# Kernel tuning notes

Measured on AMD Instinct MI355X. Metric: run time of the kernel, lower is better.

The kernel has to match this reference:

```python
import jax, jax.numpy as jnp
import numpy as np

BATCH_SIZE = 2048
TEMPERATURE = 0.5
EPS = 1e-8  # torch CosineSimilarity eps


def setup_inputs() -> dict:
    key = jax.random.key(0)
    k1, k2 = jax.random.split(key)
    d = 512
    z_i = jax.random.normal(k1, (BATCH_SIZE, d), dtype=jnp.float32)
    z_j = jax.random.normal(k2, (BATCH_SIZE, d), dtype=jnp.float32)
    return {"z_i": z_i, "z_j": z_j}


def reference(z_i, z_j):
    B = BATCH_SIZE
    n = 2 * B
    z = jnp.concatenate([z_i, z_j], axis=0)              # [n, d]
    # cosine similarity via normalize + GEMM (same math as broadcasted CosineSimilarity)
    norms = jnp.maximum(jnp.linalg.norm(z, axis=1, keepdims=True), EPS)
    zn = z / norms                                       # [n, d]
    S = zn @ zn.T                                        # [n, n]
    # drop diagonal: row i keeps columns j != i, in order (matches sim[~eye].view(n, n-1))
    cols = jnp.arange(n - 1)[None, :]                    # [1, n-1]
    rows = jnp.arange(n)[:, None]                        # [n, 1]
    idx = cols + (cols >= rows)                          # skip diagonal
    off_diag = jnp.take_along_axis(S, idx, axis=1)       # [n, n-1]
    # positive pair: pos_pairs = cat(z_j, z_i) -> partner index (i + B) mod n
    pos = jnp.take_along_axis(S, ((rows[:, 0] + B) % n)[:, None], axis=1)  # [n, 1]
    logits = jnp.concatenate([pos, off_diag], axis=1) / TEMPERATURE        # [n, n]
    # cross-entropy with label 0, reduction='sum', then / n  == mean over rows
    loss = jnp.mean(jax.nn.logsumexp(logits, axis=1) - logits[:, 0])
    return loss
```

## Files before the change

kernel.cpp:

```cpp
#include <hip/hip_runtime.h>
#include <hip/hip_bf16.h>

#define N_TOT 4096
#define D     512
#define BHALF 2048

#define EXP2_SCALE 2.8853900817779268f

typedef __attribute__((ext_vector_type(8))) short short8;
typedef __attribute__((ext_vector_type(4))) float floatx4;

__global__ void normalize_kernel(const float* __restrict__ z_i,
                                 const float* __restrict__ z_j,
                                 short* __restrict__ zn) {
    int row = blockIdx.x;
    const float* src = (row < BHALF) ? (z_i + (size_t)row * D)
                                     : (z_j + (size_t)(row - BHALF) * D);
    int t = threadIdx.x;
    float4 v = ((const float4*)src)[t];
    float ss = v.x*v.x + v.y*v.y + v.z*v.z + v.w*v.w;
    for (int off = 32; off > 0; off >>= 1) ss += __shfl_down(ss, off);
    __shared__ float red[2];
    if ((t & 63) == 0) red[t >> 6] = ss;
    __syncthreads();
    float total = red[0] + red[1];
    float inv = 1.0f / fmaxf(sqrtf(total), 1e-8f);
    short4 o;
    o.x = (short)__bfloat16_as_ushort(__float2bfloat16(v.x * inv));
    o.y = (short)__bfloat16_as_ushort(__float2bfloat16(v.y * inv));
    o.z = (short)__bfloat16_as_ushort(__float2bfloat16(v.z * inv));
    o.w = (short)__bfloat16_as_ushort(__float2bfloat16(v.w * inv));
    ((short4*)(zn + (size_t)row * D))[t] = o;
}

__launch_bounds__(256)
__global__ void gemm_fused(const short* __restrict__ zn,
                           float* __restrict__ rowsum,
                           float* __restrict__ sii,
                           float* __restrict__ spos) {
    __shared__ short At[128 * 32];
    __shared__ short Bt[128 * 32];
    const int i0 = blockIdx.x * 128;
    const int j0 = blockIdx.y * 128;
    const int t = threadIdx.x;
    const int lane = t & 63, wave = t >> 6;
    const int wm = wave & 1, wn = wave >> 1;
    const int quad = lane >> 4, l16 = lane & 15;

    floatx4 acc[4][4] = {};

    for (int kt = 0; kt < D / 32; ++kt) {
        const int k0 = kt * 32;
        #pragma unroll
        for (int it = 0; it < 2; ++it) {
            int c  = t + it * 256;
            int r  = c >> 2;
            int c8 = (c & 3) * 8;
            short8 av = *(const short8*)(zn + (size_t)(i0 + r) * D + k0 + c8);
            short8 bv = *(const short8*)(zn + (size_t)(j0 + r) * D + k0 + c8);
            *(short8*)(At + r * 32 + c8) = av;
            *(short8*)(Bt + r * 32 + c8) = bv;
        }
        __syncthreads();

        short8 af[4], bf[4];
        #pragma unroll
        for (int tm = 0; tm < 4; ++tm)
            af[tm] = *(const short8*)(At + (wm*64 + tm*16 + l16) * 32 + quad*8);
        #pragma unroll
        for (int tn = 0; tn < 4; ++tn)
            bf[tn] = *(const short8*)(Bt + (wn*64 + tn*16 + l16) * 32 + quad*8);
        #pragma unroll
        for (int tm = 0; tm < 4; ++tm)
            #pragma unroll
            for (int tn = 0; tn < 4; ++tn)
                acc[tm][tn] = __builtin_amdgcn_mfma_f32_16x16x32_bf16(
                    af[tm], bf[tn], acc[tm][tn], 0, 0, 0);
        __syncthreads();
    }

    #pragma unroll
    for (int tm = 0; tm < 4; ++tm) {
        float rs[4] = {0.f, 0.f, 0.f, 0.f};
        #pragma unroll
        for (int tn = 0; tn < 4; ++tn) {
            int gj = j0 + wn*64 + tn*16 + l16;
            #pragma unroll
            for (int r = 0; r < 4; ++r) {
                int gi = i0 + wm*64 + tm*16 + quad*4 + r;
                float s = acc[tm][tn][r];
                float e = exp2f(s * EXP2_SCALE);
                rs[r] += e;
                if (gj == gi)            sii[gi]  = s;
                if (gj == (gi ^ BHALF))  spos[gi] = s;
            }
        }
        #pragma unroll
        for (int r = 0; r < 4; ++r) {
            float v = rs[r];
            v += __shfl_xor(v, 1);
            v += __shfl_xor(v, 2);
            v += __shfl_xor(v, 4);
            v += __shfl_xor(v, 8);
            if (l16 == 0) {
                int gi = i0 + wm*64 + tm*16 + quad*4 + r;
                atomicAdd(&rowsum[gi], v);
            }
        }
    }
}

__global__ void finalize_kernel(const float* __restrict__ rowsum,
                                const float* __restrict__ sii,
                                const float* __restrict__ spos,
                                float* __restrict__ out) {
    int t = threadIdx.x;
    float acc = 0.f;
    for (int i = t; i < N_TOT; i += 256) {
        float sp = spos[i];
        float denom = rowsum[i] - exp2f(sii[i] * EXP2_SCALE)
                                + exp2f(sp     * EXP2_SCALE);
        acc += __logf(denom) - 2.0f * sp;
    }
    for (int off = 32; off > 0; off >>= 1) acc += __shfl_down(acc, off);
    __shared__ float red[4];
    if ((t & 63) == 0) red[t >> 6] = acc;
    __syncthreads();
    if (t == 0) out[0] = (red[0] + red[1] + red[2] + red[3]) / (float)N_TOT;
}

extern "C" void kernel_launch(void* const* d_in, const int* in_sizes, int n_in,
                              void* d_out, int out_size, void* d_ws, size_t ws_size,
                              hipStream_t stream) {
    const float* z_i = (const float*)d_in[0];
    const float* z_j = (const float*)d_in[1];
    float* out = (float*)d_out;

    char* ws = (char*)d_ws;
    short* zn     = (short*)ws;
    float* rowsum = (float*)(ws + (size_t)N_TOT * D * 2);
    float* sii    = rowsum + N_TOT;
    float* spos   = sii + N_TOT;

    hipMemsetAsync(rowsum, 0, N_TOT * sizeof(float), stream);

    normalize_kernel<<<N_TOT, 128, 0, stream>>>(z_i, z_j, zn);
    dim3 grid(N_TOT / 128, N_TOT / 128);
    gemm_fused<<<grid, 256, 0, stream>>>(zn, rowsum, sii, spos);
    finalize_kernel<<<1, 256, 0, stream>>>(rowsum, sii, spos, out);
}
```

Baseline: 105.0 us.

## Exploit similarity symmetry with upper-triangular tiles and direct global-to-LDS loads

The GEMM now runs only the upper-triangular 128x128 tile pairs, since the similarity matrix is symmetric. Each off-diagonal tile adds column sums into rowsum as well as row sums, roughly halving MFMA and exp work. Tile staging uses global_load_lds to copy straight into shared memory without passing through registers, and zeroing rowsum moves into the normalize kernel, which drops the memset. In exchange the column-sum reductions double the atomics per tile, and the tile-index decode is a serial loop.

New measurement: 98.49 us. 6.2% less time.

```diff
diff --git a/kernel.cpp b/kernel.cpp
--- a/kernel.cpp
+++ b/kernel.cpp
@@ -10,13 +10,18 @@
 typedef __attribute__((ext_vector_type(8))) short short8;
 typedef __attribute__((ext_vector_type(4))) float floatx4;
 
+#define AS_GLOBAL(p) ((const __attribute__((address_space(1))) void*)(p))
+#define AS_LDS(p)    ((__attribute__((address_space(3))) void*)(p))
+
 __global__ void normalize_kernel(const float* __restrict__ z_i,
                                  const float* __restrict__ z_j,
-                                 short* __restrict__ zn) {
+                                 short* __restrict__ zn,
+                                 float* __restrict__ rowsum) {
     int row = blockIdx.x;
     const float* src = (row < BHALF) ? (z_i + (size_t)row * D)
                                      : (z_j + (size_t)(row - BHALF) * D);
     int t = threadIdx.x;
+    if (t == 0) rowsum[row] = 0.0f;
     float4 v = ((const float4*)src)[t];
     float ss = v.x*v.x + v.y*v.y + v.z*v.z + v.w*v.w;
     for (int off = 32; off > 0; off >>= 1) ss += __shfl_down(ss, off);
@@ -40,8 +45,13 @@
                            float* __restrict__ spos) {
     __shared__ short At[128 * 32];
     __shared__ short Bt[128 * 32];
-    const int i0 = blockIdx.x * 128;
-    const int j0 = blockIdx.y * 128;
+
+    int b = blockIdx.x, bi = 0, rowlen = 32;
+    while (b >= rowlen) { b -= rowlen; rowlen--; bi++; }
+    const int bj = bi + b;
+    const int i0 = bi * 128;
+    const int j0 = bj * 128;
+
     const int t = threadIdx.x;
     const int lane = t & 63, wave = t >> 6;
     const int wm = wave & 1, wn = wave >> 1;
@@ -49,18 +59,23 @@
 
     floatx4 acc[4][4] = {};
 
+    const int sr = lane >> 2;
+    const int sc = (lane & 3) * 8;
+    const short* gA0 = zn + (size_t)(i0 + wave * 32 + sr)      * D + sc;
+    const short* gA1 = zn + (size_t)(i0 + wave * 32 + 16 + sr) * D + sc;
+    const short* gB0 = zn + (size_t)(j0 + wave * 32 + sr)      * D + sc;
+    const short* gB1 = zn + (size_t)(j0 + wave * 32 + 16 + sr) * D + sc;
+    short* lA0 = At + (wave * 32)      * 32;
+    short* lA1 = At + (wave * 32 + 16) * 32;
+    short* lB0 = Bt + (wave * 32)      * 32;
+    short* lB1 = Bt + (wave * 32 + 16) * 32;
+
     for (int kt = 0; kt < D / 32; ++kt) {
-        const int k0 = kt * 32;
-        #pragma unroll
-        for (int it = 0; it < 2; ++it) {
-            int c  = t + it * 256;
-            int r  = c >> 2;
-            int c8 = (c & 3) * 8;
-            short8 av = *(const short8*)(zn + (size_t)(i0 + r) * D + k0 + c8);
-            short8 bv = *(const short8*)(zn + (size_t)(j0 + r) * D + k0 + c8);
-            *(short8*)(At + r * 32 + c8) = av;
-            *(short8*)(Bt + r * 32 + c8) = bv;
-        }
+        __builtin_amdgcn_global_load_lds(AS_GLOBAL(gA0), AS_LDS(lA0), 16, 0, 0);
+        __builtin_amdgcn_global_load_lds(AS_GLOBAL(gA1), AS_LDS(lA1), 16, 0, 0);
+        __builtin_amdgcn_global_load_lds(AS_GLOBAL(gB0), AS_LDS(lB0), 16, 0, 0);
+        __builtin_amdgcn_global_load_lds(AS_GLOBAL(gB1), AS_LDS(lB1), 16, 0, 0);
+        gA0 += 32; gA1 += 32; gB0 += 32; gB1 += 32;
         __syncthreads();
 
         short8 af[4], bf[4];
@@ -79,6 +94,7 @@
         __syncthreads();
     }
 
+    float cs[4] = {0.f, 0.f, 0.f, 0.f};
     #pragma unroll
     for (int tm = 0; tm < 4; ++tm) {
         float rs[4] = {0.f, 0.f, 0.f, 0.f};
@@ -91,8 +107,9 @@
                 float s = acc[tm][tn][r];
                 float e = exp2f(s * EXP2_SCALE);
                 rs[r] += e;
-                if (gj == gi)            sii[gi]  = s;
-                if (gj == (gi ^ BHALF))  spos[gi] = s;
+                cs[tn] += e;
+                if (gj == gi)            sii[gi] = s;
+                if (gj == (gi ^ BHALF)) { spos[gi] = s; spos[gj] = s; }
             }
         }
         #pragma unroll
@@ -105,6 +122,18 @@
             if (l16 == 0) {
                 int gi = i0 + wm*64 + tm*16 + quad*4 + r;
                 atomicAdd(&rowsum[gi], v);
+            }
+        }
+    }
+    if (bi != bj) {
+        #pragma unroll
+        for (int tn = 0; tn < 4; ++tn) {
+            float v = cs[tn];
+            v += __shfl_xor(v, 16);
+            v += __shfl_xor(v, 32);
+            if (quad == 0) {
+                int gj = j0 + wn*64 + tn*16 + l16;
+                atomicAdd(&rowsum[gj], v);
             }
         }
     }
@@ -142,10 +171,7 @@
     float* sii    = rowsum + N_TOT;
     float* spos   = sii + N_TOT;
 
-    hipMemsetAsync(rowsum, 0, N_TOT * sizeof(float), stream);
-
-    normalize_kernel<<<N_TOT, 128, 0, stream>>>(z_i, z_j, zn);
-    dim3 grid(N_TOT / 128, N_TOT / 128);
-    gemm_fused<<<grid, 256, 0, stream>>>(zn, rowsum, sii, spos);
+    normalize_kernel<<<N_TOT, 128, 0, stream>>>(z_i, z_j, zn, rowsum);
+    gemm_fused<<<(32 * 33) / 2, 256, 0, stream>>>(zn, rowsum, sii, spos);
     finalize_kernel<<<1, 256, 0, stream>>>(rowsum, sii, spos, out);
 }
```
